# Kernel tuning notes

Hardware: AMD Instinct MI355X
Metric: run time of the kernel (lower is better)

## Reference

```python
import jax, jax.numpy as jnp
import numpy as np

LN_EPS = 1e-5  # torch.nn.LayerNorm default


def setup_inputs() -> dict:
    key = jax.random.key(0)
    ks = jax.random.split(key, 6)
    b, e, c, h, w, m = 4, 16, 256, 32, 64, 1024
    return {
        "x": jax.random.normal(ks[0], (b, e, c, h, w), dtype=jnp.float32),
        "ln_w": jnp.ones((c, h, w), dtype=jnp.float32),
        "ln_b": jnp.zeros((c, h, w), dtype=jnp.float32),
        "w_in": jax.random.normal(ks[1], (c, m), dtype=jnp.float32) * (1.0 / np.sqrt(c)),
        "b_in": jax.random.normal(ks[2], (m,), dtype=jnp.float32) * 0.01,
        "w_out": jax.random.normal(ks[3], (m, c), dtype=jnp.float32) * (1.0 / np.sqrt(m)),
        "b_out": jax.random.normal(ks[4], (c,), dtype=jnp.float32) * 0.01,
        "gamma": jnp.full((c,), 1e-6, dtype=jnp.float32),
    }


def reference(x, ln_w, ln_b, w_in, b_in, w_out, b_out, gamma):
    # LayerNorm over the last 3 dims (c, h, w) with affine params of shape (c, h, w)
    mu = jnp.mean(x, axis=(-3, -2, -1), keepdims=True)
    var = jnp.var(x, axis=(-3, -2, -1), keepdims=True)  # biased, matches torch
    y = (x - mu) * jax.lax.rsqrt(var + LN_EPS)
    y = y * ln_w + ln_b  # broadcast (c,h,w) over (b,e,...)

    # b e c h w -> b e h w c
    y = jnp.moveaxis(y, 2, -1)
    t = jax.nn.gelu(y @ w_in + b_in, approximate=False)  # torch GELU is exact erf
    t = (t @ w_out + b_out) * gamma  # layer scale on channel dim

    # b e h w c -> b e c h w, residual add
    return x + jnp.moveaxis(t, -1, 2)
```

## Files before the change

### kernel.cpp

```cpp
#include <hip/hip_runtime.h>
#include <math.h>

#define NS 64
#define CD 256
#define HW 2048
#define MD 1024
#define SAMPLE (CD * HW)
#define LN_EPS 1e-5f

#define PB 64
#define MC 32
#define NCH (MD / MC)

typedef float f32x4 __attribute__((ext_vector_type(4)));
typedef long i64;

__device__ __forceinline__ int swz(int p) {
  int k = (p ^ (p >> 2)) & 15;
  return ((k & 7) << 4) | (k & 8);
}

__device__ __forceinline__ void gl_lds16(const unsigned char* g, unsigned char* l) {
  __builtin_amdgcn_global_load_lds(
      (const __attribute__((address_space(1))) unsigned char*)g,
      (__attribute__((address_space(3))) unsigned char*)l, 16, 0, 0);
}

__global__ __launch_bounds__(256) void k_prep_stats(
    const float* __restrict__ x, const float* __restrict__ w_in,
    const float* __restrict__ w_out, unsigned char* __restrict__ w_in8p,
    unsigned char* __restrict__ w_out8p, double* __restrict__ partial) {
  if (blockIdx.x < 512) {
    int s = blockIdx.x >> 3, sl = blockIdx.x & 7;
    const float4* p = (const float4*)(x + (size_t)s * SAMPLE + (size_t)sl * 65536);
    double sum = 0.0, ssq = 0.0;
    for (int i = 0; i < 64; ++i) {
      float4 v = p[i * 256 + threadIdx.x];
      sum += (double)v.x + (double)v.y + (double)v.z + (double)v.w;
      ssq += (double)v.x * v.x + (double)v.y * v.y + (double)v.z * v.z + (double)v.w * v.w;
    }
    for (int off = 32; off; off >>= 1) {
      sum += __shfl_down(sum, off);
      ssq += __shfl_down(ssq, off);
    }
    __shared__ double red[4][2];
    int wv = threadIdx.x >> 6, ln = threadIdx.x & 63;
    if (ln == 0) { red[wv][0] = sum; red[wv][1] = ssq; }
    __syncthreads();
    if (threadIdx.x == 0) {
      for (int i = 1; i < 4; ++i) { sum += red[i][0]; ssq += red[i][1]; }
      partial[blockIdx.x * 2] = sum;
      partial[blockIdx.x * 2 + 1] = ssq;
    }
  } else {
    int id = (blockIdx.x - 512) * 256 + threadIdx.x;
    if (id < 65536) {
      int i = id;
      int f = i >> 7, l = (i >> 1) & 63, j0 = (i & 1) * 4;
      int m = (f >> 3) * 16 + (l & 15);
      int c0 = (f & 7) * 32 + (l >> 4) * 8 + j0;
      float a = w_in[(size_t)(c0 + 0) * MD + m];
      float b = w_in[(size_t)(c0 + 1) * MD + m];
      float c = w_in[(size_t)(c0 + 2) * MD + m];
      float d = w_in[(size_t)(c0 + 3) * MD + m];
      int r = __builtin_amdgcn_cvt_pk_fp8_f32(a, b, 0, false);
      r = __builtin_amdgcn_cvt_pk_fp8_f32(c, d, r, true);
      ((int*)w_in8p)[i] = r;
    } else {
      int i = id - 65536;
      int g = i >> 7, l = (i >> 1) & 63, j0 = (i & 1) * 4;
      int c = (g & 15) * 16 + (l & 15);
      int m0 = (g >> 4) * 32 + (l >> 4) * 8 + j0;
      float a = w_out[(size_t)(m0 + 0) * CD + c];
      float b = w_out[(size_t)(m0 + 1) * CD + c];
      float cc = w_out[(size_t)(m0 + 2) * CD + c];
      float d = w_out[(size_t)(m0 + 3) * CD + c];
      int r = __builtin_amdgcn_cvt_pk_fp8_f32(a, b, 0, false);
      r = __builtin_amdgcn_cvt_pk_fp8_f32(cc, d, r, true);
      ((int*)w_out8p)[i] = r;
    }
  }
}

__global__ void k_stats2(const double* __restrict__ partial, float* __restrict__ stats) {
  int s = threadIdx.x;
  double sum = 0.0, ssq = 0.0;
  for (int i = 0; i < 8; ++i) {
    sum += partial[(s * 8 + i) * 2];
    ssq += partial[(s * 8 + i) * 2 + 1];
  }
  double mean = sum / (double)SAMPLE;
  double var = ssq / (double)SAMPLE - mean * mean;
  stats[s * 2] = (float)mean;
  stats[s * 2 + 1] = (float)(1.0 / sqrt(var + (double)LN_EPS));
}

__global__ __launch_bounds__(512, 6) void k_fused(
    const float* __restrict__ x, const float* __restrict__ ln_w, const float* __restrict__ ln_b,
    const float* __restrict__ b_in, const float* __restrict__ b_out, const float* __restrict__ gamma,
    const unsigned char* __restrict__ w_in8p, const unsigned char* __restrict__ w_out8p,
    const float* __restrict__ stats, float* __restrict__ out) {
  __shared__ unsigned char smem[45056];
  unsigned char* Ysh = smem + 8192;

  const int tid = threadIdx.x;
  const int lane = tid & 63, l15 = lane & 15, l4 = lane >> 4;
  const int wv = tid >> 6;
  const int q = wv >> 1, h = wv & 1;
  const int s = blockIdx.x >> 5;
  const int p0 = (blockIdx.x & 31) * PB;
  const float mu = stats[s * 2], rstd = stats[s * 2 + 1];
  const float a_ln = rstd, c_ln = -mu * rstd;
  const size_t xbase = (size_t)s * SAMPLE;

  gl_lds16(w_in8p + wv * 1024 + lane * 16, smem + 24576 + wv * 1024);
  gl_lds16(w_out8p + wv * 1024 + lane * 16, smem + wv * 1024);

  #pragma unroll
  for (int it = 0; it < 2; ++it) {
    int bid = it * 512 + tid;
    int c0 = (bid >> 4) * 4, pp = (bid & 15) * 4;
    float yv[4][4];
    #pragma unroll
    for (int i = 0; i < 4; ++i) {
      size_t off = (size_t)(c0 + i) * HW + p0 + pp;
      float4 xv = *(const float4*)(x + xbase + off);
      float4 lw = *(const float4*)(ln_w + off);
      float4 lb = *(const float4*)(ln_b + off);
      yv[i][0] = fmaf(fmaf(xv.x, a_ln, c_ln), lw.x, lb.x);
      yv[i][1] = fmaf(fmaf(xv.y, a_ln, c_ln), lw.y, lb.y);
      yv[i][2] = fmaf(fmaf(xv.z, a_ln, c_ln), lw.z, lb.z);
      yv[i][3] = fmaf(fmaf(xv.w, a_ln, c_ln), lw.w, lb.w);
    }
    #pragma unroll
    for (int j = 0; j < 4; ++j) {
      int p = pp + j;
      int r = __builtin_amdgcn_cvt_pk_fp8_f32(yv[0][j], yv[1][j], 0, false);
      r = __builtin_amdgcn_cvt_pk_fp8_f32(yv[2][j], yv[3][j], r, true);
      *(int*)&Ysh[p * 256 + (c0 ^ swz(p))] = r;
    }
  }

  const int strip = q * 16;
  const int pY = strip + l15;
  const int sY = swz(pY);
  f32x4 acc2[8] = {};

  __syncthreads();

  i64 breg[8];
  #pragma unroll
  for (int kk = 0; kk < 8; ++kk)
    breg[kk] = *(const i64*)&Ysh[pY * 256 + ((kk * 32 + l4 * 8) ^ sY)];

  __syncthreads();

  const int exw = ((((h * 16 + l4 * 4) >> 3) ^ (l15 >> 2)) << 3) + ((l4 & 1) * 4);
  const int exw_off = 40960 + q * 512 + l15 * 32 + exw;
  const int exr_off = 40960 + q * 512 + l15 * 32 + ((l4 ^ (l15 >> 2)) << 3);

  for (int ch = 0; ch < NCH; ++ch) {
    if (ch) __syncthreads();

    if (ch + 1 < NCH) {
      const size_t co = (size_t)(ch + 1) * 8192;
      gl_lds16(w_in8p + co + wv * 1024 + lane * 16,
               smem + 24576 + ((ch + 1) & 1) * 8192 + wv * 1024);
      gl_lds16(w_out8p + co + wv * 1024 + lane * 16,
               smem + ((ch + 1) % 3) * 8192 + wv * 1024);
    }

    i64 a2 = 0;
    if (ch) a2 = *(const i64*)(smem + ((ch - 1) & 1) * 2048 + exr_off);

    const unsigned char* W1 = smem + 24576 + (ch & 1) * 8192;
    f32x4 acc1a = {}, acc1b = {};
    __builtin_amdgcn_s_setprio(1);
    #pragma unroll
    for (int kk = 0; kk < 4; ++kk) {
      i64 a = *(const i64*)&W1[(h * 8 + kk) * 512 + lane * 8];
      i64 b = *(const i64*)&W1[(h * 8 + 4 + kk) * 512 + lane * 8];
      acc1a = __builtin_amdgcn_mfma_f32_16x16x32_fp8_fp8(a, breg[kk], acc1a, 0, 0, 0);
      acc1b = __builtin_amdgcn_mfma_f32_16x16x32_fp8_fp8(b, breg[4 + kk], acc1b, 0, 0, 0);
    }
    __builtin_amdgcn_s_setprio(0);

    {
      const float4 bi = *(const float4*)&b_in[ch * 32 + h * 16 + l4 * 4];
      float g[4];
      #pragma unroll
      for (int r = 0; r < 4; ++r) {
        float t = acc1a[r] + acc1b[r] + ((const float*)&bi)[r];
        g[r] = t * __builtin_amdgcn_rcpf(1.0f + __expf(-1.702f * t));
      }
      int pk = __builtin_amdgcn_cvt_pk_fp8_f32(g[0], g[1], 0, false);
      pk = __builtin_amdgcn_cvt_pk_fp8_f32(g[2], g[3], pk, true);
      *(int*)(smem + (ch & 1) * 2048 + exw_off) = pk;
    }

    if (ch) {
      const unsigned char* W2 = smem + ((ch - 1) % 3) * 8192;
      __builtin_amdgcn_s_setprio(1);
      #pragma unroll
      for (int cti = 0; cti < 8; ++cti) {
        i64 b2 = *(const i64*)&W2[(h * 8 + cti) * 512 + lane * 8];
        acc2[cti] = __builtin_amdgcn_mfma_f32_16x16x32_fp8_fp8(a2, b2, acc2[cti], 0, 0, 0);
      }
      __builtin_amdgcn_s_setprio(0);
    }
  }

  __syncthreads();
  {
    const i64 a2 = *(const i64*)(smem + ((NCH - 1) & 1) * 2048 + exr_off);
    const unsigned char* W2 = smem + ((NCH - 1) % 3) * 8192;
    #pragma unroll
    for (int cti = 0; cti < 8; ++cti) {
      i64 b2 = *(const i64*)&W2[(h * 8 + cti) * 512 + lane * 8];
      acc2[cti] = __builtin_amdgcn_mfma_f32_16x16x32_fp8_fp8(a2, b2, acc2[cti], 0, 0, 0);
    }
  }

  #pragma unroll
  for (int cti = 0; cti < 8; ++cti) {
    int cc = h * 128 + cti * 16 + l15;
    float gm = gamma[cc], bo = b_out[cc];
    int p = p0 + strip + l4 * 4;
    size_t off = xbase + (size_t)cc * HW + p;
    float4 xv = *(const float4*)(x + off);
    float4 o;
    #pragma unroll
    for (int r = 0; r < 4; ++r)
      ((float*)&o)[r] = ((const float*)&xv)[r] + gm * (acc2[cti][r] + bo);
    *(float4*)(out + off) = o;
  }
}

extern "C" void kernel_launch(void* const* d_in, const int* in_sizes, int n_in,
                              void* d_out, int out_size, void* d_ws, size_t ws_size,
                              hipStream_t stream) {
  const float* x = (const float*)d_in[0];
  const float* ln_w = (const float*)d_in[1];
  const float* ln_b = (const float*)d_in[2];
  const float* w_in = (const float*)d_in[3];
  const float* b_in = (const float*)d_in[4];
  const float* w_out = (const float*)d_in[5];
  const float* b_out = (const float*)d_in[6];
  const float* gamma = (const float*)d_in[7];
  float* out = (float*)d_out;

  char* ws = (char*)d_ws;
  unsigned char* w_in8p = (unsigned char*)ws;
  unsigned char* w_out8p = (unsigned char*)(ws + 262144);
  double* partial = (double*)(ws + 524288);
  float* stats = (float*)(ws + 524288 + 8192);

  k_prep_stats<<<1024, 256, 0, stream>>>(x, w_in, w_out, w_in8p, w_out8p, partial);
  k_stats2<<<1, 64, 0, stream>>>(partial, stats);

  k_fused<<<2048, 512, 0, stream>>>(x, ln_w, ln_b, b_in, b_out, gamma,
                                    w_in8p, w_out8p, stats, out);
}
```

Before: 173.8 us.

## Load fp8 weight fragments directly from global into registers instead of LDS staging

Drops the global_load_lds double and triple buffering of the w_in and w_out fp8 tiles. Each wave now reads its MFMA weight fragments straight from global memory, relying on L2/L1 because the weights are shared across all blocks. This shrinks LDS from 44KB to 20KB, which may let more blocks fit per CU, and removes one barrier. In exchange there is no explicit prefetch, so global load latency lands on the MFMA critical path each chunk.

```diff
diff --git a/kernel.cpp b/kernel.cpp
--- a/kernel.cpp
+++ b/kernel.cpp
@@ -18,12 +18,6 @@
 __device__ __forceinline__ int swz(int p) {
   int k = (p ^ (p >> 2)) & 15;
   return ((k & 7) << 4) | (k & 8);
-}
-
-__device__ __forceinline__ void gl_lds16(const unsigned char* g, unsigned char* l) {
-  __builtin_amdgcn_global_load_lds(
-      (const __attribute__((address_space(1))) unsigned char*)g,
-      (__attribute__((address_space(3))) unsigned char*)l, 16, 0, 0);
 }
 
 __global__ __launch_bounds__(256) void k_prep_stats(
@@ -100,8 +94,8 @@
     const float* __restrict__ b_in, const float* __restrict__ b_out, const float* __restrict__ gamma,
     const unsigned char* __restrict__ w_in8p, const unsigned char* __restrict__ w_out8p,
     const float* __restrict__ stats, float* __restrict__ out) {
-  __shared__ unsigned char smem[45056];
-  unsigned char* Ysh = smem + 8192;
+  __shared__ unsigned char smem[20480];
+  unsigned char* Ysh = smem;
 
   const int tid = threadIdx.x;
   const int lane = tid & 63, l15 = lane & 15, l4 = lane >> 4;
@@ -113,9 +107,6 @@
   const float a_ln = rstd, c_ln = -mu * rstd;
   const size_t xbase = (size_t)s * SAMPLE;
 
-  gl_lds16(w_in8p + wv * 1024 + lane * 16, smem + 24576 + wv * 1024);
-  gl_lds16(w_out8p + wv * 1024 + lane * 16, smem + wv * 1024);
-
   #pragma unroll
   for (int it = 0; it < 2; ++it) {
     int bid = it * 512 + tid;
@@ -153,37 +144,39 @@
   for (int kk = 0; kk < 8; ++kk)
     breg[kk] = *(const i64*)&Ysh[pY * 256 + ((kk * 32 + l4 * 8) ^ sY)];
 
-  __syncthreads();
-
   const int exw = ((((h * 16 + l4 * 4) >> 3) ^ (l15 >> 2)) << 3) + ((l4 & 1) * 4);
-  const int exw_off = 40960 + q * 512 + l15 * 32 + exw;
-  const int exr_off = 40960 + q * 512 + l15 * 32 + ((l4 ^ (l15 >> 2)) << 3);
+  const int exw_off = 16384 + q * 512 + l15 * 32 + exw;
+  const int exr_off = 16384 + q * 512 + l15 * 32 + ((l4 ^ (l15 >> 2)) << 3);
+
+  const unsigned char* W1g = w_in8p + (size_t)h * 8 * 512 + lane * 8;
+  const unsigned char* W2g = w_out8p + (size_t)h * 8 * 512 + lane * 8;
 
   for (int ch = 0; ch < NCH; ++ch) {
     if (ch) __syncthreads();
 
-    if (ch + 1 < NCH) {
-      const size_t co = (size_t)(ch + 1) * 8192;
-      gl_lds16(w_in8p + co + wv * 1024 + lane * 16,
-               smem + 24576 + ((ch + 1) & 1) * 8192 + wv * 1024);
-      gl_lds16(w_out8p + co + wv * 1024 + lane * 16,
-               smem + ((ch + 1) % 3) * 8192 + wv * 1024);
-    }
-
     i64 a2 = 0;
-    if (ch) a2 = *(const i64*)(smem + ((ch - 1) & 1) * 2048 + exr_off);
-
-    const unsigned char* W1 = smem + 24576 + (ch & 1) * 8192;
+    if (ch) a2 = *(const i64*)(smem + exr_off + ((ch - 1) & 1) * 2048);
+
+    i64 w1f[8];
+    #pragma unroll
+    for (int kk = 0; kk < 8; ++kk)
+      w1f[kk] = *(const i64*)(W1g + (size_t)ch * 8192 + kk * 512);
+
     f32x4 acc1a = {}, acc1b = {};
     __builtin_amdgcn_s_setprio(1);
     #pragma unroll
     for (int kk = 0; kk < 4; ++kk) {
-      i64 a = *(const i64*)&W1[(h * 8 + kk) * 512 + lane * 8];
-      i64 b = *(const i64*)&W1[(h * 8 + 4 + kk) * 512 + lane * 8];
-      acc1a = __builtin_amdgcn_mfma_f32_16x16x32_fp8_fp8(a, breg[kk], acc1a, 0, 0, 0);
-      acc1b = __builtin_amdgcn_mfma_f32_16x16x32_fp8_fp8(b, breg[4 + kk], acc1b, 0, 0, 0);
+      acc1a = __builtin_amdgcn_mfma_f32_16x16x32_fp8_fp8(w1f[kk], breg[kk], acc1a, 0, 0, 0);
+      acc1b = __builtin_amdgcn_mfma_f32_16x16x32_fp8_fp8(w1f[4 + kk], breg[4 + kk], acc1b, 0, 0, 0);
     }
     __builtin_amdgcn_s_setprio(0);
+
+    i64 w2f[8];
+    if (ch) {
+      #pragma unroll
+      for (int cti = 0; cti < 8; ++cti)
+        w2f[cti] = *(const i64*)(W2g + (size_t)(ch - 1) * 8192 + cti * 512);
+    }
 
     {
       const float4 bi = *(const float4*)&b_in[ch * 32 + h * 16 + l4 * 4];
@@ -195,28 +188,24 @@
       }
       int pk = __builtin_amdgcn_cvt_pk_fp8_f32(g[0], g[1], 0, false);
       pk = __builtin_amdgcn_cvt_pk_fp8_f32(g[2], g[3], pk, true);
-      *(int*)(smem + (ch & 1) * 2048 + exw_off) = pk;
+      *(int*)(smem + exw_off + (ch & 1) * 2048) = pk;
     }
 
     if (ch) {
-      const unsigned char* W2 = smem + ((ch - 1) % 3) * 8192;
       __builtin_amdgcn_s_setprio(1);
       #pragma unroll
-      for (int cti = 0; cti < 8; ++cti) {
-        i64 b2 = *(const i64*)&W2[(h * 8 + cti) * 512 + lane * 8];
-        acc2[cti] = __builtin_amdgcn_mfma_f32_16x16x32_fp8_fp8(a2, b2, acc2[cti], 0, 0, 0);
-      }
+      for (int cti = 0; cti < 8; ++cti)
+        acc2[cti] = __builtin_amdgcn_mfma_f32_16x16x32_fp8_fp8(a2, w2f[cti], acc2[cti], 0, 0, 0);
       __builtin_amdgcn_s_setprio(0);
     }
   }
 
   __syncthreads();
   {
-    const i64 a2 = *(const i64*)(smem + ((NCH - 1) & 1) * 2048 + exr_off);
-    const unsigned char* W2 = smem + ((NCH - 1) % 3) * 8192;
+    const i64 a2 = *(const i64*)(smem + exr_off + ((NCH - 1) & 1) * 2048);
     #pragma unroll
     for (int cti = 0; cti < 8; ++cti) {
-      i64 b2 = *(const i64*)&W2[(h * 8 + cti) * 512 + lane * 8];
+      i64 b2 = *(const i64*)(W2g + (size_t)(NCH - 1) * 8192 + cti * 512);
       acc2[cti] = __builtin_amdgcn_mfma_f32_16x16x32_fp8_fp8(a2, b2, acc2[cti], 0, 0, 0);
     }
   }
```

New measurement: 422.1 us. +142.9%, slower.

## Fold stats finalize into fused kernel and repack fp8 weights for 16-byte LDS reads

Applied to the files above, without the earlier changes.

Removes the single-block k_stats2 launch: each fused block now reduces the 8 per-sample partial sums and computes mean and rstd itself. The prep kernel writes the fp8 weight tiles in a new layout, so each wave reads two MFMA operands with one 16-byte LDS load instead of two 8-byte loads. This cuts a kernel launch and its serialization point, and halves the LDS read instruction count in the inner loops. The cost is redundant double-precision work per block, repeated 2048 times.

```diff
diff --git a/kernel.cpp b/kernel.cpp
--- a/kernel.cpp
+++ b/kernel.cpp
@@ -14,6 +14,7 @@
 
 typedef float f32x4 __attribute__((ext_vector_type(4)));
 typedef long i64;
+typedef long i64x2 __attribute__((ext_vector_type(2)));
 
 __device__ __forceinline__ int swz(int p) {
   int k = (p ^ (p >> 2)) & 15;
@@ -54,52 +55,49 @@
     }
   } else {
     int id = (blockIdx.x - 512) * 256 + threadIdx.x;
+    int off = id << 2;
+    int ch = off >> 13, r = off & 8191;
+    int h = r >> 12; r &= 4095;
+    int pr = r >> 10; r &= 1023;
+    int lane = r >> 4; r &= 15;
+    int lo = r >> 3, j0 = r & 7;
+    int kk = pr * 2 + lo;
     if (id < 65536) {
-      int i = id;
-      int f = i >> 7, l = (i >> 1) & 63, j0 = (i & 1) * 4;
-      int m = (f >> 3) * 16 + (l & 15);
-      int c0 = (f & 7) * 32 + (l >> 4) * 8 + j0;
+      int m = ch * 32 + h * 16 + (lane & 15);
+      int c0 = kk * 32 + (lane >> 4) * 8 + j0;
       float a = w_in[(size_t)(c0 + 0) * MD + m];
       float b = w_in[(size_t)(c0 + 1) * MD + m];
       float c = w_in[(size_t)(c0 + 2) * MD + m];
       float d = w_in[(size_t)(c0 + 3) * MD + m];
-      int r = __builtin_amdgcn_cvt_pk_fp8_f32(a, b, 0, false);
-      r = __builtin_amdgcn_cvt_pk_fp8_f32(c, d, r, true);
-      ((int*)w_in8p)[i] = r;
+      int rr = __builtin_amdgcn_cvt_pk_fp8_f32(a, b, 0, false);
+      rr = __builtin_amdgcn_cvt_pk_fp8_f32(c, d, rr, true);
+      *(int*)(w_in8p + off) = rr;
     } else {
-      int i = id - 65536;
-      int g = i >> 7, l = (i >> 1) & 63, j0 = (i & 1) * 4;
-      int c = (g & 15) * 16 + (l & 15);
-      int m0 = (g >> 4) * 32 + (l >> 4) * 8 + j0;
+      off = (id - 65536) << 2;
+      ch = off >> 13; r = off & 8191;
+      h = r >> 12; r &= 4095;
+      pr = r >> 10; r &= 1023;
+      lane = r >> 4; r &= 15;
+      lo = r >> 3; j0 = r & 7;
+      int ct = pr * 2 + lo;
+      int c = h * 128 + ct * 16 + (lane & 15);
+      int m0 = ch * 32 + (lane >> 4) * 8 + j0;
       float a = w_out[(size_t)(m0 + 0) * CD + c];
       float b = w_out[(size_t)(m0 + 1) * CD + c];
       float cc = w_out[(size_t)(m0 + 2) * CD + c];
       float d = w_out[(size_t)(m0 + 3) * CD + c];
-      int r = __builtin_amdgcn_cvt_pk_fp8_f32(a, b, 0, false);
-      r = __builtin_amdgcn_cvt_pk_fp8_f32(cc, d, r, true);
-      ((int*)w_out8p)[i] = r;
-    }
-  }
-}
-
-__global__ void k_stats2(const double* __restrict__ partial, float* __restrict__ stats) {
-  int s = threadIdx.x;
-  double sum = 0.0, ssq = 0.0;
-  for (int i = 0; i < 8; ++i) {
-    sum += partial[(s * 8 + i) * 2];
-    ssq += partial[(s * 8 + i) * 2 + 1];
-  }
-  double mean = sum / (double)SAMPLE;
-  double var = ssq / (double)SAMPLE - mean * mean;
-  stats[s * 2] = (float)mean;
-  stats[s * 2 + 1] = (float)(1.0 / sqrt(var + (double)LN_EPS));
+      int rr = __builtin_amdgcn_cvt_pk_fp8_f32(a, b, 0, false);
+      rr = __builtin_amdgcn_cvt_pk_fp8_f32(cc, d, rr, true);
+      *(int*)(w_out8p + off) = rr;
+    }
+  }
 }
 
 __global__ __launch_bounds__(512, 6) void k_fused(
     const float* __restrict__ x, const float* __restrict__ ln_w, const float* __restrict__ ln_b,
     const float* __restrict__ b_in, const float* __restrict__ b_out, const float* __restrict__ gamma,
     const unsigned char* __restrict__ w_in8p, const unsigned char* __restrict__ w_out8p,
-    const float* __restrict__ stats, float* __restrict__ out) {
+    const double* __restrict__ partial, float* __restrict__ out) {
   __shared__ unsigned char smem[45056];
   unsigned char* Ysh = smem + 8192;
 
@@ -109,9 +107,18 @@
   const int q = wv >> 1, h = wv & 1;
   const int s = blockIdx.x >> 5;
   const int p0 = (blockIdx.x & 31) * PB;
-  const float mu = stats[s * 2], rstd = stats[s * 2 + 1];
-  const float a_ln = rstd, c_ln = -mu * rstd;
   const size_t xbase = (size_t)s * SAMPLE;
+
+  double sum = 0.0, ssq = 0.0;
+  #pragma unroll
+  for (int i = 0; i < 8; ++i) {
+    sum += partial[s * 16 + i * 2];
+    ssq += partial[s * 16 + i * 2 + 1];
+  }
+  double mean = sum / (double)SAMPLE;
+  double var = ssq / (double)SAMPLE - mean * mean;
+  const float rstd = (float)(1.0 / sqrt(var + (double)LN_EPS));
+  const float a_ln = rstd, c_ln = -(float)mean * rstd;
 
   gl_lds16(w_in8p + wv * 1024 + lane * 16, smem + 24576 + wv * 1024);
   gl_lds16(w_out8p + wv * 1024 + lane * 16, smem + wv * 1024);
@@ -173,15 +180,14 @@
     i64 a2 = 0;
     if (ch) a2 = *(const i64*)(smem + ((ch - 1) & 1) * 2048 + exr_off);
 
-    const unsigned char* W1 = smem + 24576 + (ch & 1) * 8192;
+    const unsigned char* W1 = smem + 24576 + (ch & 1) * 8192 + h * 4096;
     f32x4 acc1a = {}, acc1b = {};
     __builtin_amdgcn_s_setprio(1);
     #pragma unroll
-    for (int kk = 0; kk < 4; ++kk) {
-      i64 a = *(const i64*)&W1[(h * 8 + kk) * 512 + lane * 8];
-      i64 b = *(const i64*)&W1[(h * 8 + 4 + kk) * 512 + lane * 8];
-      acc1a = __builtin_amdgcn_mfma_f32_16x16x32_fp8_fp8(a, breg[kk], acc1a, 0, 0, 0);
-      acc1b = __builtin_amdgcn_mfma_f32_16x16x32_fp8_fp8(b, breg[4 + kk], acc1b, 0, 0, 0);
+    for (int kp = 0; kp < 4; ++kp) {
+      i64x2 w = *(const i64x2*)&W1[kp * 1024 + lane * 16];
+      acc1a = __builtin_amdgcn_mfma_f32_16x16x32_fp8_fp8(w.x, breg[kp * 2], acc1a, 0, 0, 0);
+      acc1b = __builtin_amdgcn_mfma_f32_16x16x32_fp8_fp8(w.y, breg[kp * 2 + 1], acc1b, 0, 0, 0);
     }
     __builtin_amdgcn_s_setprio(0);
 
@@ -199,12 +205,13 @@
     }
 
     if (ch) {
-      const unsigned char* W2 = smem + ((ch - 1) % 3) * 8192;
+      const unsigned char* W2 = smem + ((ch - 1) % 3) * 8192 + h * 4096;
       __builtin_amdgcn_s_setprio(1);
       #pragma unroll
-      for (int cti = 0; cti < 8; ++cti) {
-        i64 b2 = *(const i64*)&W2[(h * 8 + cti) * 512 + lane * 8];
-        acc2[cti] = __builtin_amdgcn_mfma_f32_16x16x32_fp8_fp8(a2, b2, acc2[cti], 0, 0, 0);
+      for (int cp = 0; cp < 4; ++cp) {
+        i64x2 w = *(const i64x2*)&W2[cp * 1024 + lane * 16];
+        acc2[cp * 2] = __builtin_amdgcn_mfma_f32_16x16x32_fp8_fp8(a2, w.x, acc2[cp * 2], 0, 0, 0);
+        acc2[cp * 2 + 1] = __builtin_amdgcn_mfma_f32_16x16x32_fp8_fp8(a2, w.y, acc2[cp * 2 + 1], 0, 0, 0);
       }
       __builtin_amdgcn_s_setprio(0);
     }
@@ -213,11 +220,12 @@
   __syncthreads();
   {
     const i64 a2 = *(const i64*)(smem + ((NCH - 1) & 1) * 2048 + exr_off);
-    const unsigned char* W2 = smem + ((NCH - 1) % 3) * 8192;
-    #pragma unroll
-    for (int cti = 0; cti < 8; ++cti) {
-      i64 b2 = *(const i64*)&W2[(h * 8 + cti) * 512 + lane * 8];
-      acc2[cti] = __builtin_amdgcn_mfma_f32_16x16x32_fp8_fp8(a2, b2, acc2[cti], 0, 0, 0);
+    const unsigned char* W2 = smem + ((NCH - 1) % 3) * 8192 + h * 4096;
+    #pragma unroll
+    for (int cp = 0; cp < 4; ++cp) {
+      i64x2 w = *(const i64x2*)&W2[cp * 1024 + lane * 16];
+      acc2[cp * 2] = __builtin_amdgcn_mfma_f32_16x16x32_fp8_fp8(a2, w.x, acc2[cp * 2], 0, 0, 0);
+      acc2[cp * 2 + 1] = __builtin_amdgcn_mfma_f32_16x16x32_fp8_fp8(a2, w.y, acc2[cp * 2 + 1], 0, 0, 0);
     }
   }
 
@@ -253,11 +261,9 @@
   unsigned char* w_in8p = (unsigned char*)ws;
   unsigned char* w_out8p = (unsigned char*)(ws + 262144);
   double* partial = (double*)(ws + 524288);
-  float* stats = (float*)(ws + 524288 + 8192);
 
   k_prep_stats<<<1024, 256, 0, stream>>>(x, w_in, w_out, w_in8p, w_out8p, partial);
-  k_stats2<<<1, 64, 0, stream>>>(partial, stats);
 
   k_fused<<<2048, 512, 0, stream>>>(x, ln_w, ln_b, b_in, b_out, gamma,
-                                    w_in8p, w_out8p, stats, out);
-}
+                                    w_in8p, w_out8p, partial, out);
+}
```

Measured after the change: 169.8 us. -2.3%, faster.
